# Optimization experiments

Measured on AMD Instinct MI355X. Metric: run time of the kernel, lower is better.

## Reference

```python
import jax, jax.numpy as jnp
import numpy as np

STOP_IX, CONTINUE_IX = 0, 1


def setup_inputs() -> dict:
    key = jax.random.key(0)
    B, T, b, A = 64, 512, 64, 18
    ks = jax.random.split(key, 5)
    # normalized log-probabilities, as produced by the abstract policy net
    stop_logps = jax.nn.log_softmax(jax.random.normal(ks[0], (B, T + 1, b, 2)), axis=-1)
    start_logps = jax.nn.log_softmax(jax.random.normal(ks[1], (B, T + 1, b)), axis=-1)
    action_logps = jax.nn.log_softmax(jax.random.normal(ks[2], (B, T + 1, b, A)), axis=-1)
    actions = jax.random.randint(ks[3], (B, T), 0, A)
    lengths = jax.random.randint(ks[4], (B,), 1, T + 1)  # traj length in [1, T]
    return dict(stop_logps=stop_logps, start_logps=start_logps,
                action_logps=action_logps, actions=actions, lengths=lengths)


def reference(stop_logps, start_logps, action_logps, actions, lengths):
    B, Tp1, b, _ = stop_logps.shape
    T = Tp1 - 1
    # chosen action logps per (batch, step, option): (B, T, b)
    chosen = jnp.take_along_axis(action_logps[:, :T], actions[:, :, None, None], axis=3)[..., 0]
    beta = stop_logps[..., STOP_IX]        # (B, T+1, b) log p(stop)
    ombeta = stop_logps[..., CONTINUE_IX]  # (B, T+1, b) log p(continue)
    eye = jnp.eye(b, dtype=bool)

    # f_0: all mass on option 0 (log prob 0)
    f0 = jnp.full((B, b), -jnp.inf, dtype=stop_logps.dtype).at[:, 0].set(0.0)

    def step(f_prev, xs):
        beta_i, ombeta_i, start_i, chosen_i = xs  # each (B, b)
        # trans[k,i,j] = logaddexp(beta_i + start_j, [i==j] * one_minus_beta_i)
        bs = beta_i[:, :, None] + start_i[:, None, :]  # (B, b, b)
        trans = jnp.where(eye[None], jnp.logaddexp(bs, ombeta_i[:, :, None]), bs)
        f_new = jax.nn.logsumexp(f_prev[:, :, None] + trans + chosen_i[:, None, :], axis=1)
        return f_new, f_new

    # per-step inputs for i = 1 .. T-1, time-major: (T-1, B, b)
    xs = (jnp.moveaxis(beta[:, 1:T], 0, 1),
          jnp.moveaxis(ombeta[:, 1:T], 0, 1),
          jnp.moveaxis(start_logps[:, 1:T], 0, 1),
          jnp.moveaxis(chosen[:, 1:T], 0, 1))
    _, fs = jax.lax.scan(step, f0, xs)
    f_all = jnp.concatenate([f0[None], fs], axis=0)  # (T, B, b)

    batch_ix = jnp.arange(B)
    x0 = f_all[lengths - 1, batch_ix]                 # (B, b)
    x1 = stop_logps[batch_ix, lengths, :, STOP_IX]    # (B, b)
    total_logps = jax.nn.logsumexp(x0 + x1, axis=1)   # (B,)
    return -jnp.sum(total_logps)
```

## Files before the change

kernel.cpp:

```cpp
#include <hip/hip_runtime.h>


#define CH   8
#define WARM 16
#define CLEN 64
#define SLOT 16

template <int CTRL, int RMASK>
__device__ __forceinline__ float dpp_add(float x) {
    int yi = __builtin_amdgcn_update_dpp(
        0, __builtin_bit_cast(int, x), CTRL, RMASK, 0xf, true);
    return x + __builtin_bit_cast(float, yi);
}

__device__ __forceinline__ float wave_sum64(float x) {
    x = dpp_add<0x111, 0xf>(x);
    x = dpp_add<0x112, 0xf>(x);
    x = dpp_add<0x114, 0xf>(x);
    x = dpp_add<0x118, 0xf>(x);
    x = dpp_add<0x142, 0xa>(x);
    x = dpp_add<0x143, 0xc>(x);
    return __builtin_bit_cast(float,
        __builtin_amdgcn_readlane(__builtin_bit_cast(int, x), 63));
}

__global__ __launch_bounds__(64)
void hmm_fwd(const float* __restrict__ stop,
             const float* __restrict__ start,
             const float* __restrict__ act,
             const int*   __restrict__ actions,
             const int*   __restrict__ lengths,
             float* __restrict__ ws,
             int T, int A)
{
    const int bi   = blockIdx.x;
    const int c    = blockIdx.y;
    const int lane = threadIdx.x;
    const int Tp1  = T + 1;
    const int NB   = 64;
    const int rowA = NB * A;

    const int L = lengths[bi];
    const int a = 1 + c * CLEN;
    const int cstar = (L >= 2) ? ((L - 2) / CLEN) : 0;
    if (c > cstar) return;

    const int t_end = min(L, a + CLEN);
    const int t0    = (c == 0) ? 1 : (a - WARM);
    const int n     = t_end - t0;
    const int nwarm = a - t0;

    const float* stopB  = stop  + (size_t)bi * Tp1 * NB * 2;
    const float* startB = start + (size_t)bi * Tp1 * NB;
    const float* actB   = act   + (size_t)bi * Tp1 * NB * A;
    const int*   actsB  = actions + (size_t)bi * T;

    __shared__ int offL[CLEN + WARM + CH];
    for (int i = lane; i < n + CH; i += 64) {
        const int tt = min(t0 + i, t_end - 1);
        offL[i] = tt * rowA + actsB[tt];
    }

    float p = (c == 0) ? ((lane == 0) ? 1.0f : 0.0f) : 1.0f;
    float slast   = 1.0f;
    float warmcap = 0.0f;
    float Eshift  = 0.0f;

    const float* spL = stopB  + (size_t)t0 * (NB * 2) + lane * 2;
    const float* stL = startB + (size_t)t0 * NB + lane;
    const int laneA = lane * A;

    float bB[2][CH], bO[2][CH], bS[2][CH], bC[2][CH];

#define LOADF(SL, j) do {                                                    \
    const float* sp  = spL + (size_t)(j) * (CH * NB * 2);                    \
    const float* st2 = stL + (size_t)(j) * (CH * NB);                        \
    _Pragma("unroll")                                                        \
    for (int i = 0; i < CH; ++i) {                                           \
        bC[SL][i] = actB[offL[(j) * CH + i] + laneA];                        \
        const float2 so = *(const float2*)(sp + i * (NB * 2));               \
        bB[SL][i] = so.x;                                                    \
        bO[SL][i] = so.y;                                                    \
        bS[SL][i] = st2[i * NB];                                             \
    } } while (0)

#define LOADC(SL, j) do {                                                    \
    _Pragma("unroll")                                                        \
    for (int i = 0; i < CH; ++i) {                                           \
        bC[SL][i] = actB[offL[(j) * CH + i] + laneA];                        \
        const int tt = min(t0 + (j) * CH + i, t_end - 1);                    \
        const float2 so = *(const float2*)(stopB + (size_t)tt * (NB * 2)     \
                                           + lane * 2);                      \
        bB[SL][i] = so.x;                                                    \
        bO[SL][i] = so.y;                                                    \
        bS[SL][i] = startB[(size_t)tt * NB + lane];                          \
    } } while (0)

#define LOAD(SL, j) do {                                                     \
    if (((j) + 1) * CH <= n) LOADF(SL, j); else LOADC(SL, j); } while (0)

#define COMPUTE(SL, j) do {                                                  \
    _Pragma("unroll")                                                        \
    for (int i = 0; i < CH; ++i) {                                           \
        if ((j) * CH + i < n) {                                              \
            const float e1 = __expf(bC[SL][i] + bS[SL][i]);                  \
            const float e2 = __expf(bC[SL][i] + bO[SL][i]);                  \
            const float eb = __expf(bB[SL][i]);                              \
            const float q  = e2 * p;                 \
            const float s  = wave_sum64(p * eb);                             \
            slast = s;                                                       \
            if ((j) * CH + i == nwarm - 1)                                   \
                warmcap = __log2f(s) + Eshift;                               \
            p = fmaf(e1, s, q);                                              \
        }                                                                    \
    }                                                                        \
                                  \
    {                                                                        \
        const unsigned sb = __builtin_bit_cast(unsigned, slast);             \
        const int ef = (int)(sb >> 23);                 \
        const float sc = __builtin_bit_cast(float,                           \
                             (unsigned)(254 - ef) << 23);   \
        p *= sc;                                                             \
        slast *= sc;                                                         \
        Eshift += (float)(ef - 127);                                         \
    } } while (0)

    const int nch = (n + CH - 1) / CH;
    if (n > 0) {
        int j = 0;
        LOAD(0, 0);
        while (true) {
            if (j + 1 < nch) LOAD(1, j + 1);
            COMPUTE(0, j);
            ++j; if (j >= nch) break;
            if (j + 1 < nch) LOAD(0, j + 1);
            COMPUTE(1, j);
            ++j; if (j >= nch) break;
        }
    }

    float C2;
    if (c == cstar) {
        const float bl = stopB[(size_t)L * (NB * 2) + lane * 2];
        const float s  = wave_sum64(p * __expf(bl));
        C2 = __log2f(s) + Eshift - warmcap;
    } else {
        C2 = __log2f(slast) + Eshift - warmcap;
    }

    if (lane == 0)
        atomicAdd(ws + bi * SLOT, C2);

#undef LOADF
#undef LOADC
#undef LOAD
#undef COMPUTE
}

__global__ __launch_bounds__(64)
void hmm_reduce(const float* __restrict__ ws, float* __restrict__ out, int B)
{
    const int lane = threadIdx.x;
    float v = (lane < B) ? ws[lane * SLOT] : 0.0f;
    const float s = wave_sum64(v);
    if (lane == 0)
        out[0] = -0.69314718055994531f * s;
}

extern "C" void kernel_launch(void* const* d_in, const int* in_sizes, int n_in,
                              void* d_out, int out_size, void* d_ws, size_t ws_size,
                              hipStream_t stream)
{
    const float* stop    = (const float*)d_in[0];
    const float* start   = (const float*)d_in[1];
    const float* act     = (const float*)d_in[2];
    const int*   actions = (const int*)d_in[3];
    const int*   lengths = (const int*)d_in[4];
    float* out = (float*)d_out;
    float* ws  = (float*)d_ws;

    const int B   = in_sizes[4];
    const int T   = in_sizes[3] / B;
    const int Tp1 = T + 1;
    const int A   = in_sizes[2] / (B * Tp1 * 64);

    const int NC = (T - 1 + CLEN - 1) / CLEN;

    (void)hipMemsetAsync(ws, 0, (size_t)B * SLOT * sizeof(float), stream);
    hmm_fwd<<<dim3(B, NC), dim3(64), 0, stream>>>(stop, start, act, actions,
                                                  lengths, ws, T, A);
    hmm_reduce<<<dim3(1), dim3(64), 0, stream>>>(ws, out, B);
}
```

Baseline: 218.3 us.

## Precompute exponentiated transition terms in a parallel prep kernel

Adds a fully parallel prep kernel that gathers the chosen action logp and writes exp(chosen+start), exp(chosen+continue) and exp(stop) to workspace for every (batch, step, option). The serial forward recurrence then only loads these precomputed values, which removes the exps and the scattered action gather from its critical path. The atomic accumulation and memset are replaced by per-chunk slot writes that the reduce kernel sums. In exchange there is an extra kernel launch, about 25 MB of workspace writes and reads, and exp work is now done for every step, including steps beyond each trajectory's length.

Result: slower. 249.0 us (+14.1%).

```diff
diff --git a/kernel.cpp b/kernel.cpp
--- a/kernel.cpp
+++ b/kernel.cpp
@@ -4,7 +4,7 @@
 #define CH   8
 #define WARM 16
 #define CLEN 64
-#define SLOT 16
+#define NB   64
 
 template <int CTRL, int RMASK>
 __device__ __forceinline__ float dpp_add(float x) {
@@ -24,76 +24,86 @@
         __builtin_amdgcn_readlane(__builtin_bit_cast(int, x), 63));
 }
 
+__global__ __launch_bounds__(256)
+void hmm_prep(const float* __restrict__ stop,
+              const float* __restrict__ start,
+              const float* __restrict__ act,
+              const int*   __restrict__ actions,
+              float* __restrict__ pe12,
+              float* __restrict__ peb,
+              int T, int A, int N)
+{
+    const int idx = blockIdx.x * 256 + threadIdx.x;
+    if (idx >= N) return;
+    const int k  = idx & 63;
+    const int bt = idx >> 6;
+    const int b  = bt / T;
+    const int t  = bt - b * T;
+    const size_t btk = ((size_t)b * (T + 1) + t) * NB + k;
+
+    const int   a  = actions[bt];
+    const float ch = act[btk * A + a];
+    const float st = start[btk];
+    const float2 so = *(const float2*)(stop + btk * 2);
+
+    const size_t o = (size_t)bt * NB + k;
+    ((float2*)pe12)[o] = make_float2(__expf(ch + st), __expf(ch + so.y));
+    peb[o] = __expf(so.x);
+}
+
 __global__ __launch_bounds__(64)
 void hmm_fwd(const float* __restrict__ stop,
-             const float* __restrict__ start,
-             const float* __restrict__ act,
-             const int*   __restrict__ actions,
-             const int*   __restrict__ lengths,
-             float* __restrict__ ws,
-             int T, int A)
+             const float2* __restrict__ pe12,
+             const float*  __restrict__ peb,
+             const int*    __restrict__ lengths,
+             float* __restrict__ slots,
+             int T, int NC)
 {
     const int bi   = blockIdx.x;
     const int c    = blockIdx.y;
     const int lane = threadIdx.x;
-    const int Tp1  = T + 1;
-    const int NB   = 64;
-    const int rowA = NB * A;
 
     const int L = lengths[bi];
-    const int a = 1 + c * CLEN;
     const int cstar = (L >= 2) ? ((L - 2) / CLEN) : 0;
-    if (c > cstar) return;
-
+    if (c > cstar) {
+        if (lane == 0) slots[bi * NC + c] = 0.0f;
+        return;
+    }
+
+    const int a     = 1 + c * CLEN;
     const int t_end = min(L, a + CLEN);
     const int t0    = (c == 0) ? 1 : (a - WARM);
     const int n     = t_end - t0;
     const int nwarm = a - t0;
 
-    const float* stopB  = stop  + (size_t)bi * Tp1 * NB * 2;
-    const float* startB = start + (size_t)bi * Tp1 * NB;
-    const float* actB   = act   + (size_t)bi * Tp1 * NB * A;
-    const int*   actsB  = actions + (size_t)bi * T;
-
-    __shared__ int offL[CLEN + WARM + CH];
-    for (int i = lane; i < n + CH; i += 64) {
-        const int tt = min(t0 + i, t_end - 1);
-        offL[i] = tt * rowA + actsB[tt];
-    }
+    const float2* q12 = pe12 + ((size_t)bi * T + t0) * NB + lane;
+    const float*  qeb = peb  + ((size_t)bi * T + t0) * NB + lane;
 
     float p = (c == 0) ? ((lane == 0) ? 1.0f : 0.0f) : 1.0f;
     float slast   = 1.0f;
     float warmcap = 0.0f;
     float Eshift  = 0.0f;
 
-    const float* spL = stopB  + (size_t)t0 * (NB * 2) + lane * 2;
-    const float* stL = startB + (size_t)t0 * NB + lane;
-    const int laneA = lane * A;
-
-    float bB[2][CH], bO[2][CH], bS[2][CH], bC[2][CH];
+    float bE1[2][CH], bE2[2][CH], bEb[2][CH];
 
 #define LOADF(SL, j) do {                                                    \
-    const float* sp  = spL + (size_t)(j) * (CH * NB * 2);                    \
-    const float* st2 = stL + (size_t)(j) * (CH * NB);                        \
     _Pragma("unroll")                                                        \
     for (int i = 0; i < CH; ++i) {                                           \
-        bC[SL][i] = actB[offL[(j) * CH + i] + laneA];                        \
-        const float2 so = *(const float2*)(sp + i * (NB * 2));               \
-        bB[SL][i] = so.x;                                                    \
-        bO[SL][i] = so.y;                                                    \
-        bS[SL][i] = st2[i * NB];                                             \
+        const float2 v = q12[((j) * CH + i) * NB];                           \
+        bE1[SL][i] = v.x;                                                    \
+        bE2[SL][i] = v.y;                                                    \
+        bEb[SL][i] = qeb[((j) * CH + i) * NB];                               \
     } } while (0)
 
 #define LOADC(SL, j) do {                                                    \
     _Pragma("unroll")                                                        \
     for (int i = 0; i < CH; ++i) {                                           \
-        bC[SL][i] = actB[offL[(j) * CH + i] + laneA];                        \
         const int tt = min(t0 + (j) * CH + i, t_end - 1);                    \
-        const float2 so = *(const float2*)(stopB + (size_t)tt * (NB * 2)     \
-                                           + lane * 2);                      \
-        bB[SL][i] = so.x;                                                    \
-        bO[SL][i] = so.y;                                                    \
-        bS[SL][i] = startB[(size_t)tt * NB + lane];                          \
+        const size_t o = ((size_t)bi * T + tt) * NB + lane;                  \
+        const float2 v = pe12[o];                                            \
+        bE1[SL][i] = v.x;                                                    \
+        bE2[SL][i] = v.y;                                                    \
+        bEb[SL][i] = peb[o];                                                 \
     } } while (0)
 
 #define LOAD(SL, j) do {                                                     \
@@ -103,23 +113,19 @@
     _Pragma("unroll")                                                        \
     for (int i = 0; i < CH; ++i) {                                           \
         if ((j) * CH + i < n) {                                              \
-            const float e1 = __expf(bC[SL][i] + bS[SL][i]);                  \
-            const float e2 = __expf(bC[SL][i] + bO[SL][i]);                  \
-            const float eb = __expf(bB[SL][i]);                              \
-            const float q  = e2 * p;                 \
-            const float s  = wave_sum64(p * eb);                             \
+            const float q = bE2[SL][i] * p;          \
+            const float s = wave_sum64(p * bEb[SL][i]);                      \
             slast = s;                                                       \
             if ((j) * CH + i == nwarm - 1)                                   \
                 warmcap = __log2f(s) + Eshift;                               \
-            p = fmaf(e1, s, q);                                              \
+            p = fmaf(bE1[SL][i], s, q);                                      \
         }                                                                    \
     }                                                                        \
-                                  \
-    {                                                                        \
+    {                             \
         const unsigned sb = __builtin_bit_cast(unsigned, slast);             \
-        const int ef = (int)(sb >> 23);                 \
+        const int ef = (int)(sb >> 23);                                      \
         const float sc = __builtin_bit_cast(float,                           \
-                             (unsigned)(254 - ef) << 23);   \
+                             (unsigned)(254 - ef) << 23);                    \
         p *= sc;                                                             \
         slast *= sc;                                                         \
         Eshift += (float)(ef - 127);                                         \
@@ -141,7 +147,7 @@
 
     float C2;
     if (c == cstar) {
-        const float bl = stopB[(size_t)L * (NB * 2) + lane * 2];
+        const float bl = stop[(((size_t)bi * (T + 1) + L) * NB + lane) * 2];
         const float s  = wave_sum64(p * __expf(bl));
         C2 = __log2f(s) + Eshift - warmcap;
     } else {
@@ -149,7 +155,7 @@
     }
 
     if (lane == 0)
-        atomicAdd(ws + bi * SLOT, C2);
+        slots[bi * NC + c] = C2;
 
 #undef LOADF
 #undef LOADC
@@ -158,10 +164,11 @@
 }
 
 __global__ __launch_bounds__(64)
-void hmm_reduce(const float* __restrict__ ws, float* __restrict__ out, int B)
+void hmm_reduce(const float* __restrict__ slots, float* __restrict__ out, int M)
 {
     const int lane = threadIdx.x;
-    float v = (lane < B) ? ws[lane * SLOT] : 0.0f;
+    float v = 0.0f;
+    for (int i = lane; i < M; i += 64) v += slots[i];
     const float s = wave_sum64(v);
     if (lane == 0)
         out[0] = -0.69314718055994531f * s;
@@ -177,17 +184,21 @@
     const int*   actions = (const int*)d_in[3];
     const int*   lengths = (const int*)d_in[4];
     float* out = (float*)d_out;
-    float* ws  = (float*)d_ws;
 
     const int B   = in_sizes[4];
     const int T   = in_sizes[3] / B;
     const int Tp1 = T + 1;
     const int A   = in_sizes[2] / (B * Tp1 * 64);
-
-    const int NC = (T - 1 + CLEN - 1) / CLEN;
-
-    (void)hipMemsetAsync(ws, 0, (size_t)B * SLOT * sizeof(float), stream);
-    hmm_fwd<<<dim3(B, NC), dim3(64), 0, stream>>>(stop, start, act, actions,
-                                                  lengths, ws, T, A);
-    hmm_reduce<<<dim3(1), dim3(64), 0, stream>>>(ws, out, B);
-}
+    const int NC  = (T - 1 + CLEN - 1) / CLEN;
+
+    float* pe12  = (float*)d_ws;
+    float* peb   = pe12 + (size_t)B * T * NB * 2;
+    float* slots = peb  + (size_t)B * T * NB;
+
+    const int N = B * T * NB;
+    hmm_prep<<<dim3((N + 255) / 256), dim3(256), 0, stream>>>(
+        stop, start, act, actions, pe12, peb, T, A, N);
+    hmm_fwd<<<dim3(B, NC), dim3(64), 0, stream>>>(
+        stop, (const float2*)pe12, peb, lengths, slots, T, NC);
+    hmm_reduce<<<dim3(1), dim3(64), 0, stream>>>(slots, out, B * NC);
+}
```
